# Kernel tuning notes

Hardware: AMD Instinct MI355X
Metric: run time of the kernel (lower is better)

## Reference

```python
import jax, jax.numpy as jnp
import numpy as np

N, E, F, H, L, G, C = 50000, 800000, 64, 128, 4, 64, 10
GAMMA = 10.0  # Gaussian RBF width for centers in (0,1)
CENTERS = jnp.linspace(0.0, 1.0, H)


def _ssp(v):
    # shifted softplus, SchNet's nonlinearity
    return jax.nn.softplus(v) - 0.6931472


def setup_inputs() -> dict:
    key = jax.random.key(0)
    ks = jax.random.split(key, 20)

    def w(k, shape, fan_in):
        return (jax.random.normal(k, shape, dtype=jnp.float32) / np.sqrt(fan_in)).astype(jnp.float32)

    x = jax.random.normal(ks[0], (N, F), dtype=jnp.float32)
    edge_dist = jax.random.uniform(ks[1], (E,), dtype=jnp.float32)
    edge_src = jax.random.randint(ks[2], (E,), 0, N, dtype=jnp.int32)
    edge_dst = jax.random.randint(ks[3], (E,), 0, N, dtype=jnp.int32)
    graph_ids = jnp.sort(jax.random.randint(ks[4], (N,), 0, G, dtype=jnp.int32))

    return {
        "x": x, "edge_dist": edge_dist,
        "edge_src": edge_src, "edge_dst": edge_dst, "graph_ids": graph_ids,
        # first-layer node projection F->H, remaining layers H->H (stacked)
        "W1_0": w(ks[5], (F, H), F), "b1_0": jnp.zeros((H,), jnp.float32),
        "W1_rest": w(ks[6], (L - 1, H, H), H), "b1_rest": jnp.zeros((L - 1, H), jnp.float32),
        # filter-generating MLP on RBF features, per layer
        "Wf1": w(ks[7], (L, H, H), H), "bf1": jnp.zeros((L, H), jnp.float32),
        "Wf2": w(ks[8], (L, H, H), H), "bf2": jnp.zeros((L, H), jnp.float32),
        # output projection per layer
        "W2": w(ks[9], (L, H, H), H), "b2": jnp.zeros((L, H), jnp.float32),
        # readout FC
        "fc_w": w(ks[10], (H, C), H), "fc_b": jnp.zeros((C,), jnp.float32),
    }


def _schnet_conv(x, rbf, src, dst, W1, b1, Wf1, bf1, Wf2, bf2, W2, b2):
    # CFConv: project nodes, gate gathered source features with a distance
    # filter, scatter-sum to destinations, project out.
    filt = _ssp(rbf @ Wf1 + bf1) @ Wf2 + bf2          # [E, H]
    h = x @ W1 + b1                                    # [N, H]
    msg = h[src] * filt                                # [E, H] gather + gate
    agg = jax.ops.segment_sum(msg, dst, num_segments=N)  # [N, H] scatter-sum
    return agg @ W2 + b2


def reference(x, edge_dist, edge_src, edge_dst, graph_ids,
              W1_0, b1_0, W1_rest, b1_rest, Wf1, bf1, Wf2, bf2, W2, b2,
              fc_w, fc_b):
    # Gaussian radial basis expansion of edge distances, shared across layers
    rbf = jnp.exp(-GAMMA * (edge_dist[:, None] - CENTERS) ** 2)  # [E, H]

    h = jax.nn.relu(_schnet_conv(x, rbf, edge_src, edge_dst,
                                 W1_0, b1_0, Wf1[0], bf1[0], Wf2[0], bf2[0],
                                 W2[0], b2[0]))
    for i in range(L - 1):
        h = jax.nn.relu(_schnet_conv(h, rbf, edge_src, edge_dst,
                                     W1_rest[i], b1_rest[i],
                                     Wf1[i + 1], bf1[i + 1],
                                     Wf2[i + 1], bf2[i + 1],
                                     W2[i + 1], b2[i + 1]))

    # dgl.mean_nodes: per-graph mean over nodes
    sums = jax.ops.segment_sum(h, graph_ids, num_segments=G)           # [G, H]
    cnts = jax.ops.segment_sum(jnp.ones((N,), h.dtype), graph_ids, num_segments=G)
    pooled = sums / jnp.maximum(cnts, 1.0)[:, None]

    logits = pooled @ fc_w + fc_b                                       # [G, C]
    return jax.nn.log_softmax(logits, axis=1)
```

## Files before the change

### kernel.cpp

```cpp
#include <hip/hip_runtime.h>
#include <math.h>

#define NN 50000
#define EE 800000
#define FF 64
#define HH 128
#define LL 4
#define GG 64
#define CC 10
#define TT 512
#define TTP 513
#define BD 64
#define ABLK 1024
#define EPB 782
#define SEGC 192
#define SUBB 96
#define SRW 6250

#define PB_CVTW 8
#define PB_TAB ((TT / 16) * LL)
#define PB_CVTX (NN * FF / 4 / 256)
#define PB_PART ABLK

#define SCB (8 * SUBB)
#define GEMMB (NN / 16)

typedef unsigned short ushort_t;
typedef unsigned int uint_t;
typedef unsigned long long u64_t;

typedef short s8v __attribute__((ext_vector_type(8)));
typedef float f32x4 __attribute__((ext_vector_type(4)));

__device__ inline ushort_t f2bf(float f) {
  uint_t u = __float_as_uint(f);
  uint_t r = (u + 0x7FFFu + ((u >> 16) & 1u)) >> 16;
  return (ushort_t)r;
}
__device__ inline float bf1f(ushort_t v) { return __uint_as_float(((uint_t)v) << 16); }

__device__ inline ushort_t f2h(float f) {
  union { _Float16 h[2]; ushort_t us[2]; } c;
  c.h[0] = (_Float16)f;
  return c.us[0];
}
__device__ inline float h_lo(uint_t u) {
  union { uint_t w; _Float16 h[2]; } c; c.w = u; return (float)c.h[0];
}
__device__ inline float h_hi(uint_t u) {
  union { uint_t w; _Float16 h[2]; } c; c.w = u; return (float)c.h[1];
}

__global__ __launch_bounds__(256) void prep(
    const float* __restrict__ x, ushort_t* __restrict__ xb,
    const float* __restrict__ W1_0, const float* __restrict__ W1_rest,
    const float* __restrict__ W2, ushort_t* __restrict__ wt,
    const float* __restrict__ Wf1, const float* __restrict__ bf1,
    const float* __restrict__ Wf2, const float* __restrict__ bf2,
    ushort_t* __restrict__ tables,
    const int* __restrict__ dst, const int* __restrict__ src,
    const float* __restrict__ dist,
    uint_t* __restrict__ seg, int* __restrict__ segcnt, int* __restrict__ bcnt,
    const int* __restrict__ gid, int* __restrict__ gcnt, float* __restrict__ gsum) {
  __shared__ float rbf[16][HH];
  __shared__ float hid[16][HH];
  __shared__ int lcnt[8];
  int tid = threadIdx.x;
  int b = blockIdx.x;

  if (b < PB_CVTW) {
    int mid = b;
    const float* srcm; int K;
    if (mid == 0) { srcm = W1_0; K = FF; }
    else if (mid < 4) { srcm = W1_rest + (size_t)(mid - 1) * HH * HH; K = HH; }
    else { srcm = W2 + (size_t)(mid - 4) * HH * HH; K = HH; }
    ushort_t* dstm = wt + (size_t)mid * HH * HH;
    for (int idx = tid; idx < K * HH; idx += 256) {
      int k = idx >> 7, n = idx & 127;
      __builtin_nontemporal_store(f2bf(srcm[idx]), &dstm[n * K + k]);
    }
  } else if (b < PB_CVTW + PB_TAB) {
    int bb = b - PB_CVTW;
    int l = bb & 3;
    int tb = (bb >> 2) * 16;
    int j = tid & 127;
    float c = j * (1.0f / (HH - 1));
#pragma unroll
    for (int tt2 = 0; tt2 < 16; ++tt2) {
      float d = (tb + tt2) * (1.0f / (TT - 1));
      float dd = d - c;
      rbf[tt2][j] = expf(-10.0f * dd * dd);
    }
    __syncthreads();
    const float* W1f = Wf1 + (size_t)l * HH * HH;
    float s[16];
    float bb1 = bf1[l * HH + j];
#pragma unroll
    for (int tt2 = 0; tt2 < 16; ++tt2) s[tt2] = bb1;
    for (int k = 0; k < HH; ++k) {
      float wk = W1f[(size_t)k * HH + j];
#pragma unroll
      for (int tt2 = 0; tt2 < 16; ++tt2) s[tt2] += rbf[tt2][k] * wk;
    }
#pragma unroll
    for (int tt2 = 0; tt2 < 16; ++tt2)
      hid[tt2][j] = fmaxf(s[tt2], 0.f) + log1pf(expf(-fabsf(s[tt2]))) - 0.6931472f;
    __syncthreads();
    const float* W2f = Wf2 + (size_t)l * HH * HH;
    float bb2 = bf2[l * HH + j];
#pragma unroll
    for (int tt2 = 0; tt2 < 16; ++tt2) s[tt2] = bb2;
    for (int k = 0; k < HH; ++k) {
      float wk = W2f[(size_t)k * HH + j];
#pragma unroll
      for (int tt2 = 0; tt2 < 16; ++tt2) s[tt2] += hid[tt2][k] * wk;
    }
    if (tid < 128) {
#pragma unroll
      for (int tt2 = 0; tt2 < 16; ++tt2)
        __builtin_nontemporal_store(f2h(s[tt2]),
                                    &tables[((size_t)l * TTP + 1 + tb + tt2) * HH + j]);
    }
  } else if (b < PB_CVTW + PB_TAB + PB_CVTX) {
    int i = (b - PB_CVTW - PB_TAB) * 256 + tid;
    const float4* x4 = (const float4*)x;
    float4 v = x4[i];
    union { ushort_t us[4]; u64_t u; } pk;
    pk.us[0] = f2bf(v.x); pk.us[1] = f2bf(v.y); pk.us[2] = f2bf(v.z); pk.us[3] = f2bf(v.w);
    __builtin_nontemporal_store(pk.u, (u64_t*)&xb[i * 4]);
  } else if (b < PB_CVTW + PB_TAB + PB_CVTX + PB_PART) {
    int pb = b - PB_CVTW - PB_TAB - PB_CVTX;
    if (tid < 8) lcnt[tid] = 0;
    int z = pb * 49 + tid;
    if (tid < 49 && z < NN) bcnt[z] = 0;
    __syncthreads();
    int e0 = pb * EPB;
    int e1 = min(e0 + EPB, EE);
    for (int e = e0 + tid; e < e1; e += 256) {
      int d = __builtin_nontemporal_load(dst + e);
      int s = __builtin_nontemporal_load(src + e);
      float di = __builtin_nontemporal_load(dist + e);
      float u = di * (float)(TT - 1);
      int t0 = (int)(fminf(fmaxf(u, 0.f), (float)(TT - 1)) + 0.5f);
      if (t0 > TT - 1) t0 = TT - 1;
      int r = d / SRW;
      int pos = atomicAdd(&lcnt[r], 1);
      if (pos < SEGC) {
        uint_t* sp = seg + (((size_t)(r << 10) + pb) * SEGC + pos) * 2;
        __builtin_nontemporal_store((uint_t)d, sp);
        __builtin_nontemporal_store(((uint_t)s << 10) | (uint_t)(t0 + 1), sp + 1);
      }
    }
    __syncthreads();
    if (tid < 8) segcnt[(tid << 10) + pb] = min(lcnt[tid], SEGC);
  } else {
    for (int i = tid; i < GG * HH; i += 256) gsum[i] = 0.f;
    for (int i = tid; i < LL * HH; i += 256)
      __builtin_nontemporal_store((ushort_t)0,
                                  &tables[(size_t)(i >> 7) * TTP * HH + (i & 127)]);
    if (tid < GG) {
      int g = tid;
      int lo = 0, hi = NN;
      while (lo < hi) { int m = (lo + hi) >> 1; if (gid[m] < g) lo = m + 1; else hi = m; }
      int b0 = lo;
      lo = 0; hi = NN;
      int g1 = g + 1;
      while (lo < hi) { int m = (lo + hi) >> 1; if (gid[m] < g1) lo = m + 1; else hi = m; }
      gcnt[g] = lo - b0;
    }
  }
}

__global__ __launch_bounds__(256) void scatter_gemm1(
    const uint_t* __restrict__ seg, const int* __restrict__ segcnt,
    int* __restrict__ bcnt, uint_t* __restrict__ epad,
    const ushort_t* __restrict__ xb, const ushort_t* __restrict__ wt,
    const float* __restrict__ b1_0, ushort_t* __restrict__ pbuf) {
  int tid = threadIdx.x;
  if (blockIdx.x < SCB) {
    int r = blockIdx.x & 7;
    int sub = blockIdx.x >> 3;
    for (int b = sub; b < ABLK; b += SUBB) {
      int cnt = segcnt[(r << 10) + b];
      const uint_t* sp = seg + ((size_t)(r << 10) + b) * SEGC * 2;
      for (int i = tid; i < cnt; i += 256) {
        uint_t ex = __builtin_nontemporal_load(sp + i * 2);
        uint_t ey = __builtin_nontemporal_load(sp + i * 2 + 1);
        int slot = atomicAdd(&bcnt[ex], 1);
        if (slot < BD) __builtin_nontemporal_store(ey, &epad[(size_t)ex * BD + slot]);
      }
    }
  } else {
    int tile = blockIdx.x - SCB;
    int lane = tid & 63, wave = tid >> 6, m = lane & 15, quad = lane >> 4;
    int rowbase = tile * 16, colbase = wave * 32;
    const ushort_t* arow = xb + (size_t)(rowbase + m) * FF;
    const ushort_t* brow0 = wt + (size_t)(colbase + m) * FF;
    const ushort_t* brow1 = wt + (size_t)(colbase + 16 + m) * FF;
    f32x4 acc0 = {0.f, 0.f, 0.f, 0.f};
    f32x4 acc1 = {0.f, 0.f, 0.f, 0.f};
    for (int kc = 0; kc < FF; kc += 32) {
      int k = kc + quad * 8;
      union { uint4 u; s8v v; } a, b0, b1;
      a.u  = *(const uint4*)(arow + k);
      b0.u = *(const uint4*)(brow0 + k);
      b1.u = *(const uint4*)(brow1 + k);
      acc0 = __builtin_amdgcn_mfma_f32_16x16x32_bf16(a.v, b0.v, acc0, 0, 0, 0);
      acc1 = __builtin_amdgcn_mfma_f32_16x16x32_bf16(a.v, b1.v, acc1, 0, 0, 0);
    }
    float bb0 = b1_0[colbase + m];
    float bb1 = b1_0[colbase + 16 + m];
#pragma unroll
    for (int reg = 0; reg < 4; ++reg) {
      int row = rowbase + quad * 4 + reg;
      __builtin_nontemporal_store(f2h(acc0[reg] + bb0), &pbuf[(size_t)row * HH + colbase + m]);
      __builtin_nontemporal_store(f2h(acc1[reg] + bb1), &pbuf[(size_t)row * HH + colbase + 16 + m]);
    }
  }
}

__global__ __launch_bounds__(512) void fused_layer(
    const ushort_t* __restrict__ pIn, const ushort_t* __restrict__ table,
    const uint_t* __restrict__ epad, const int* __restrict__ bcnt,
    const ushort_t* __restrict__ WT2, const float* __restrict__ b2l,
    const ushort_t* __restrict__ WT1, const float* __restrict__ b1l,
    ushort_t* __restrict__ OUT, int last) {
  __shared__ ushort_t At[16 * 128];
  __shared__ ushort_t T[16 * 128];
  int tid = threadIdx.x;
  int lane = tid & 63;
  int wv = tid >> 6;
  int tile = blockIdx.x;
  const uint_t* pu = (const uint_t*)pIn;
  const uint_t* tu = (const uint_t*)table;

  int baseV = tile * 16 + wv * 2;
  uint_t ed[2];
  float ax[2], ay[2];
  int B = 0;
#pragma unroll
  for (int i = 0; i < 2; ++i) {
    int n = min(bcnt[baseV + i], BD);
    ed[i] = (lane < n) ? epad[(size_t)(baseV + i) * BD + lane] : 0u;
    B = max(B, (n + 3) >> 2);
    ax[i] = 0.f; ay[i] = 0.f;
  }
  for (int c = 0; c < B; ++c) {
    uint_t pv[2][4], fv[2][4];
#pragma unroll
    for (int i = 0; i < 2; ++i) {
#pragma unroll
      for (int k = 0; k < 4; ++k) {
        uint_t e = (uint_t)__builtin_amdgcn_readlane((int)ed[i], c * 4 + k);
        pv[i][k] = pu[(size_t)(e >> 10) * 64 + lane];
        fv[i][k] = tu[(size_t)(e & 1023u) * 64 + lane];
      }
    }
#pragma unroll
    for (int i = 0; i < 2; ++i) {
#pragma unroll
      for (int k = 0; k < 4; ++k) {
        ax[i] += h_lo(pv[i][k]) * h_lo(fv[i][k]);
        ay[i] += h_hi(pv[i][k]) * h_hi(fv[i][k]);
      }
    }
  }
#pragma unroll
  for (int i = 0; i < 2; ++i) {
    int r = wv * 2 + i;
    uint_t packed = (uint_t)f2bf(ax[i]) | ((uint_t)f2bf(ay[i]) << 16);
    ((uint_t*)At)[r * 64 + (((lane >> 2) ^ r) << 2) + (lane & 3)] = packed;
  }
  __syncthreads();
  int m = lane & 15, quad = lane >> 4;
  int rowbase = tile * 16, colbase = wv * 16;
  {
    const ushort_t* brow0 = WT2 + (size_t)(colbase + m) * HH;
    f32x4 acc0 = {0.f, 0.f, 0.f, 0.f};
    for (int kc = 0; kc < HH; kc += 32) {
      int k = kc + quad * 8;
      int g = k >> 3;
      union { uint4 u; s8v v; } a, b0;
      a.u = *(const uint4*)&At[m * 128 + ((g ^ m) << 3)];
      b0.u = *(const uint4*)(brow0 + k);
      acc0 = __builtin_amdgcn_mfma_f32_16x16x32_bf16(a.v, b0.v, acc0, 0, 0, 0);
    }
    float bb0 = b2l[colbase + m];
    if (last) {
#pragma unroll
      for (int reg = 0; reg < 4; ++reg) {
        int row = rowbase + quad * 4 + reg;
        __builtin_nontemporal_store(f2bf(fmaxf(acc0[reg] + bb0, 0.f)),
                                    &OUT[(size_t)row * HH + colbase + m]);
      }
      return;
    }
#pragma unroll
    for (int reg = 0; reg < 4; ++reg) {
      int r = quad * 4 + reg;
      float v0 = fmaxf(acc0[reg] + bb0, 0.f);
      int c0 = colbase + m;
      T[r * 128 + (((c0 >> 3) ^ r) << 3) + (c0 & 7)] = f2bf(v0);
    }
  }
  __syncthreads();
  {
    const ushort_t* brow0 = WT1 + (size_t)(colbase + m) * HH;
    f32x4 acc0 = {0.f, 0.f, 0.f, 0.f};
    for (int kc = 0; kc < HH; kc += 32) {
      int k0 = kc + quad * 8;
      int g = k0 >> 3;
      union { uint4 u; s8v v; } a, b0;
      a.u = *(const uint4*)&T[m * 128 + ((g ^ m) << 3)];
      b0.u = *(const uint4*)(brow0 + k0);
      acc0 = __builtin_amdgcn_mfma_f32_16x16x32_bf16(a.v, b0.v, acc0, 0, 0, 0);
    }
    float bb0 = b1l[colbase + m];
#pragma unroll
    for (int reg = 0; reg < 4; ++reg) {
      int row = rowbase + quad * 4 + reg;
      __builtin_nontemporal_store(f2h(acc0[reg] + bb0),
                                  &OUT[(size_t)row * HH + colbase + m]);
    }
  }
}

__global__ __launch_bounds__(128) void pool_kernel(const ushort_t* __restrict__ h, const int* __restrict__ gid,
                                                   float* __restrict__ gsum) {
  int j = threadIdx.x;
  int i0 = blockIdx.x * 128;
  int i1 = min(i0 + 128, NN);
  if (i0 >= NN) return;
  float acc = 0.f;
  int gcur = gid[i0];
  for (int i = i0; i < i1; ++i) {
    int g = gid[i];
    if (g != gcur) {
      atomicAdd(&gsum[gcur * HH + j], acc);
      acc = 0.f;
      gcur = g;
    }
    acc += bf1f(h[(size_t)i * HH + j]);
  }
  atomicAdd(&gsum[gcur * HH + j], acc);
}

__global__ __launch_bounds__(128) void final_kernel(const float* __restrict__ gsum, const int* __restrict__ gcnt,
                                                    const float* __restrict__ fc_w, const float* __restrict__ fc_b,
                                                    float* __restrict__ out) {
  int g = blockIdx.x, j = threadIdx.x;
  __shared__ float pooled[HH];
  __shared__ float logits[CC];
  __shared__ float lse;
  float cnt = fmaxf((float)gcnt[g], 1.0f);
  pooled[j] = gsum[g * HH + j] / cnt;
  __syncthreads();
  if (j < CC) {
    float s = fc_b[j];
    for (int k = 0; k < HH; ++k) s += pooled[k] * fc_w[k * CC + j];
    logits[j] = s;
  }
  __syncthreads();
  if (j == 0) {
    float m = -1e30f;
    for (int c = 0; c < CC; ++c) m = fmaxf(m, logits[c]);
    float s = 0.f;
    for (int c = 0; c < CC; ++c) s += expf(logits[c] - m);
    lse = m + logf(s);
  }
  __syncthreads();
  if (j < CC) out[g * CC + j] = logits[j] - lse;
}

extern "C" void kernel_launch(void* const* d_in, const int* in_sizes, int n_in,
                              void* d_out, int out_size, void* d_ws, size_t ws_size,
                              hipStream_t stream) {
  const float* x       = (const float*)d_in[0];
  const float* edist   = (const float*)d_in[1];
  const int*   esrc    = (const int*)d_in[2];
  const int*   edst    = (const int*)d_in[3];
  const int*   gid     = (const int*)d_in[4];
  const float* W1_0    = (const float*)d_in[5];
  const float* b1_0    = (const float*)d_in[6];
  const float* W1_rest = (const float*)d_in[7];
  const float* b1_rest = (const float*)d_in[8];
  const float* Wf1     = (const float*)d_in[9];
  const float* bf1     = (const float*)d_in[10];
  const float* Wf2     = (const float*)d_in[11];
  const float* bf2     = (const float*)d_in[12];
  const float* W2      = (const float*)d_in[13];
  const float* b2      = (const float*)d_in[14];
  const float* fc_w    = (const float*)d_in[15];
  const float* fc_b    = (const float*)d_in[16];
  float* out = (float*)d_out;

  char* ws = (char*)d_ws;
  size_t o = 0;
  auto alloc = [&](size_t bytes) {
    void* p = ws + o;
    o += (bytes + 255) & ~(size_t)255;
    return p;
  };
  ushort_t* tables = (ushort_t*)alloc(sizeof(ushort_t) * (size_t)LL * TTP * HH);
  ushort_t* xb     = (ushort_t*)alloc(sizeof(ushort_t) * (size_t)NN * FF);
  ushort_t* wt     = (ushort_t*)alloc(sizeof(ushort_t) * 8 * HH * HH);
  ushort_t* pbuf   = (ushort_t*)alloc(sizeof(ushort_t) * (size_t)NN * HH);
  ushort_t* pbuf2  = (ushort_t*)alloc(sizeof(ushort_t) * (size_t)NN * HH);
  ushort_t* hbuf   = (ushort_t*)alloc(sizeof(ushort_t) * (size_t)NN * HH);
  int*      bcnt   = (int*)alloc(sizeof(int) * NN);
  uint_t*   epad   = (uint_t*)alloc(sizeof(uint_t) * (size_t)NN * BD);
  uint_t*   seg    = (uint_t*)alloc(sizeof(uint_t) * (size_t)2 * 8 * ABLK * SEGC);
  int*      segcnt = (int*)alloc(sizeof(int) * 8 * ABLK);
  float*    gsum   = (float*)alloc(sizeof(float) * GG * HH);
  int*      gcnt   = (int*)alloc(sizeof(int) * GG);

  const int prepBlocks = PB_CVTW + PB_TAB + PB_CVTX + PB_PART + 1;
  prep<<<prepBlocks, 256, 0, stream>>>(x, xb, W1_0, W1_rest, W2, wt,
                                       Wf1, bf1, Wf2, bf2, tables,
                                       edst, esrc, edist, seg, segcnt, bcnt,
                                       gid, gcnt, gsum);
  scatter_gemm1<<<SCB + GEMMB, 256, 0, stream>>>(seg, segcnt, bcnt, epad,
                                                 xb, wt, b1_0, pbuf);

  ushort_t* pIn = pbuf;
  ushort_t* pOut = pbuf2;
  for (int l = 0; l < LL; ++l) {
    int last = (l == LL - 1);
    fused_layer<<<GEMMB, 512, 0, stream>>>(
        pIn, tables + (size_t)l * TTP * HH, epad, bcnt,
        wt + (size_t)(4 + l) * HH * HH, b2 + (size_t)l * HH,
        last ? nullptr : (wt + (size_t)(1 + l) * HH * HH),
        last ? nullptr : (b1_rest + (size_t)l * HH),
        last ? hbuf : pOut, last);
    ushort_t* tmp = pIn; pIn = pOut; pOut = tmp;
  }

  pool_kernel<<<(NN + 127) / 128, 128, 0, stream>>>(hbuf, gid, gsum);
  final_kernel<<<GG, 128, 0, stream>>>(gsum, gcnt, fc_w, fc_b, out);
}
```

Measured before the change: 424.6 us.

## Quantize node features and filter tables to int8 with per-row scales

Node projection outputs and the distance filter tables are stored as int8 with one float scale per row, replacing fp16. This halves the bytes gathered per edge in the message loop. The filter table is shrunk from 512 to 256 distance bins and the edge encoding is adjusted to match. Nontemporal stores are replaced with plain stores. The cost is extra per-row max reductions, scale loads on every edge, and lower numerical precision.

Measured after the change: 436.9 us. 1.03x slower.

```diff
diff --git a/kernel.cpp b/kernel.cpp
--- a/kernel.cpp
+++ b/kernel.cpp
@@ -8,8 +8,8 @@
 #define LL 4
 #define GG 64
 #define CC 10
-#define TT 512
-#define TTP 513
+#define TT 256
+#define TTP 257
 #define BD 64
 #define ABLK 1024
 #define EPB 782
@@ -38,17 +38,10 @@
   return (ushort_t)r;
 }
 __device__ inline float bf1f(ushort_t v) { return __uint_as_float(((uint_t)v) << 16); }
-
 __device__ inline ushort_t f2h(float f) {
   union { _Float16 h[2]; ushort_t us[2]; } c;
   c.h[0] = (_Float16)f;
   return c.us[0];
-}
-__device__ inline float h_lo(uint_t u) {
-  union { uint_t w; _Float16 h[2]; } c; c.w = u; return (float)c.h[0];
-}
-__device__ inline float h_hi(uint_t u) {
-  union { uint_t w; _Float16 h[2]; } c; c.w = u; return (float)c.h[1];
 }
 
 __global__ __launch_bounds__(256) void prep(
@@ -57,7 +50,7 @@
     const float* __restrict__ W2, ushort_t* __restrict__ wt,
     const float* __restrict__ Wf1, const float* __restrict__ bf1,
     const float* __restrict__ Wf2, const float* __restrict__ bf2,
-    ushort_t* __restrict__ tables,
+    char* __restrict__ tabQ, float* __restrict__ tabS,
     const int* __restrict__ dst, const int* __restrict__ src,
     const float* __restrict__ dist,
     uint_t* __restrict__ seg, int* __restrict__ segcnt, int* __restrict__ bcnt,
@@ -65,6 +58,7 @@
   __shared__ float rbf[16][HH];
   __shared__ float hid[16][HH];
   __shared__ int lcnt[8];
+  __shared__ uint_t rmx[16];
   int tid = threadIdx.x;
   int b = blockIdx.x;
 
@@ -77,13 +71,14 @@
     ushort_t* dstm = wt + (size_t)mid * HH * HH;
     for (int idx = tid; idx < K * HH; idx += 256) {
       int k = idx >> 7, n = idx & 127;
-      __builtin_nontemporal_store(f2bf(srcm[idx]), &dstm[n * K + k]);
+      dstm[n * K + k] = f2bf(srcm[idx]);
     }
   } else if (b < PB_CVTW + PB_TAB) {
     int bb = b - PB_CVTW;
     int l = bb & 3;
     int tb = (bb >> 2) * 16;
     int j = tid & 127;
+    if (tid < 16) rmx[tid] = 0u;
     float c = j * (1.0f / (HH - 1));
 #pragma unroll
     for (int tt2 = 0; tt2 < 16; ++tt2) {
@@ -118,16 +113,25 @@
     if (tid < 128) {
 #pragma unroll
       for (int tt2 = 0; tt2 < 16; ++tt2)
-        __builtin_nontemporal_store(f2h(s[tt2]),
-                                    &tables[((size_t)l * TTP + 1 + tb + tt2) * HH + j]);
-    }
+        atomicMax(&rmx[tt2], __float_as_uint(fabsf(s[tt2])));
+    }
+    __syncthreads();
+    if (tid < 128) {
+#pragma unroll
+      for (int tt2 = 0; tt2 < 16; ++tt2) {
+        float inv = 127.0f / fmaxf(__uint_as_float(rmx[tt2]), 1e-30f);
+        tabQ[((size_t)l * TTP + 1 + tb + tt2) * HH + j] = (char)(int)rintf(s[tt2] * inv);
+      }
+    }
+    if (tid < 16)
+      tabS[(size_t)l * TTP + 1 + tb + tid] = __uint_as_float(rmx[tid]) * (1.0f / 127.0f);
   } else if (b < PB_CVTW + PB_TAB + PB_CVTX) {
     int i = (b - PB_CVTW - PB_TAB) * 256 + tid;
     const float4* x4 = (const float4*)x;
     float4 v = x4[i];
     union { ushort_t us[4]; u64_t u; } pk;
     pk.us[0] = f2bf(v.x); pk.us[1] = f2bf(v.y); pk.us[2] = f2bf(v.z); pk.us[3] = f2bf(v.w);
-    __builtin_nontemporal_store(pk.u, (u64_t*)&xb[i * 4]);
+    *(u64_t*)&xb[i * 4] = pk.u;
   } else if (b < PB_CVTW + PB_TAB + PB_CVTX + PB_PART) {
     int pb = b - PB_CVTW - PB_TAB - PB_CVTX;
     if (tid < 8) lcnt[tid] = 0;
@@ -147,8 +151,8 @@
       int pos = atomicAdd(&lcnt[r], 1);
       if (pos < SEGC) {
         uint_t* sp = seg + (((size_t)(r << 10) + pb) * SEGC + pos) * 2;
-        __builtin_nontemporal_store((uint_t)d, sp);
-        __builtin_nontemporal_store(((uint_t)s << 10) | (uint_t)(t0 + 1), sp + 1);
+        sp[0] = (uint_t)d;
+        sp[1] = ((uint_t)s << 9) | (uint_t)(t0 + 1);
       }
     }
     __syncthreads();
@@ -156,10 +160,10 @@
   } else {
     for (int i = tid; i < GG * HH; i += 256) gsum[i] = 0.f;
     for (int i = tid; i < LL * HH; i += 256)
-      __builtin_nontemporal_store((ushort_t)0,
-                                  &tables[(size_t)(i >> 7) * TTP * HH + (i & 127)]);
-    if (tid < GG) {
-      int g = tid;
+      tabQ[(size_t)(i >> 7) * TTP * HH + (i & 127)] = 0;
+    if (tid < LL) tabS[(size_t)tid * TTP] = 0.f;
+    if (tid >= 32 && tid < 32 + GG) {
+      int g = tid - 32;
       int lo = 0, hi = NN;
       while (lo < hi) { int m = (lo + hi) >> 1; if (gid[m] < g) lo = m + 1; else hi = m; }
       int b0 = lo;
@@ -175,7 +179,9 @@
     const uint_t* __restrict__ seg, const int* __restrict__ segcnt,
     int* __restrict__ bcnt, uint_t* __restrict__ epad,
     const ushort_t* __restrict__ xb, const ushort_t* __restrict__ wt,
-    const float* __restrict__ b1_0, ushort_t* __restrict__ pbuf) {
+    const float* __restrict__ b1_0, char* __restrict__ q8Out,
+    float* __restrict__ sclOut) {
+  __shared__ uint_t rmaxL[16];
   int tid = threadIdx.x;
   if (blockIdx.x < SCB) {
     int r = blockIdx.x & 7;
@@ -187,10 +193,11 @@
         uint_t ex = __builtin_nontemporal_load(sp + i * 2);
         uint_t ey = __builtin_nontemporal_load(sp + i * 2 + 1);
         int slot = atomicAdd(&bcnt[ex], 1);
-        if (slot < BD) __builtin_nontemporal_store(ey, &epad[(size_t)ex * BD + slot]);
+        if (slot < BD) epad[(size_t)ex * BD + slot] = ey;
       }
     }
   } else {
+    if (tid < 16) rmaxL[tid] = 0u;
     int tile = blockIdx.x - SCB;
     int lane = tid & 63, wave = tid >> 6, m = lane & 15, quad = lane >> 4;
     int rowbase = tile * 16, colbase = wave * 32;
@@ -210,29 +217,46 @@
     }
     float bb0 = b1_0[colbase + m];
     float bb1 = b1_0[colbase + 16 + m];
+    float v0r[4], v1r[4];
 #pragma unroll
     for (int reg = 0; reg < 4; ++reg) {
-      int row = rowbase + quad * 4 + reg;
-      __builtin_nontemporal_store(f2h(acc0[reg] + bb0), &pbuf[(size_t)row * HH + colbase + m]);
-      __builtin_nontemporal_store(f2h(acc1[reg] + bb1), &pbuf[(size_t)row * HH + colbase + 16 + m]);
-    }
+      v0r[reg] = acc0[reg] + bb0;
+      v1r[reg] = acc1[reg] + bb1;
+      int r = quad * 4 + reg;
+      atomicMax(&rmaxL[r], __float_as_uint(fmaxf(fabsf(v0r[reg]), fabsf(v1r[reg]))));
+    }
+    __syncthreads();
+#pragma unroll
+    for (int reg = 0; reg < 4; ++reg) {
+      int r = quad * 4 + reg;
+      int row = rowbase + r;
+      float inv = 127.0f / fmaxf(__uint_as_float(rmaxL[r]), 1e-30f);
+      q8Out[(size_t)row * HH + colbase + m] = (char)(int)rintf(v0r[reg] * inv);
+      q8Out[(size_t)row * HH + colbase + 16 + m] = (char)(int)rintf(v1r[reg] * inv);
+    }
+    if (tid < 16) sclOut[rowbase + tid] = __uint_as_float(rmaxL[tid]) * (1.0f / 127.0f);
   }
 }
 
 __global__ __launch_bounds__(512) void fused_layer(
-    const ushort_t* __restrict__ pIn, const ushort_t* __restrict__ table,
+    const char* __restrict__ q8In, const float* __restrict__ sclIn,
+    const char* __restrict__ tabQ, const float* __restrict__ tabS,
     const uint_t* __restrict__ epad, const int* __restrict__ bcnt,
     const ushort_t* __restrict__ WT2, const float* __restrict__ b2l,
     const ushort_t* __restrict__ WT1, const float* __restrict__ b1l,
-    ushort_t* __restrict__ OUT, int last) {
+    char* __restrict__ q8Out, float* __restrict__ sclOut,
+    ushort_t* __restrict__ hbuf, int last) {
   __shared__ ushort_t At[16 * 128];
   __shared__ ushort_t T[16 * 128];
+  __shared__ uint_t rmaxL[16];
   int tid = threadIdx.x;
   int lane = tid & 63;
   int wv = tid >> 6;
   int tile = blockIdx.x;
-  const uint_t* pu = (const uint_t*)pIn;
-  const uint_t* tu = (const uint_t*)table;
+  if (tid < 16) rmaxL[tid] = 0u;
+
+  const ushort_t* pq = (const ushort_t*)q8In;
+  const ushort_t* tq = (const ushort_t*)tabQ;
 
   int baseV = tile * 16 + wv * 2;
   uint_t ed[2];
@@ -247,21 +271,28 @@
   }
   for (int c = 0; c < B; ++c) {
     uint_t pv[2][4], fv[2][4];
+    float sc[2][4];
 #pragma unroll
     for (int i = 0; i < 2; ++i) {
 #pragma unroll
       for (int k = 0; k < 4; ++k) {
         uint_t e = (uint_t)__builtin_amdgcn_readlane((int)ed[i], c * 4 + k);
-        pv[i][k] = pu[(size_t)(e >> 10) * 64 + lane];
-        fv[i][k] = tu[(size_t)(e & 1023u) * 64 + lane];
+        pv[i][k] = pq[(size_t)(e >> 9) * 64 + lane];
+        fv[i][k] = tq[(size_t)(e & 511u) * 64 + lane];
+        sc[i][k] = sclIn[e >> 9] * tabS[e & 511u];
       }
     }
 #pragma unroll
     for (int i = 0; i < 2; ++i) {
 #pragma unroll
       for (int k = 0; k < 4; ++k) {
-        ax[i] += h_lo(pv[i][k]) * h_lo(fv[i][k]);
-        ay[i] += h_hi(pv[i][k]) * h_hi(fv[i][k]);
+        int wp = (int)pv[i][k], wf = (int)fv[i][k];
+        float p0 = (float)((wp << 24) >> 24);
+        float p1 = (float)((wp << 16) >> 24);
+        float f0 = (float)((wf << 24) >> 24);
+        float f1 = (float)((wf << 16) >> 24);
+        ax[i] += (p0 * f0) * sc[i][k];
+        ay[i] += (p1 * f1) * sc[i][k];
       }
     }
   }
@@ -290,8 +321,7 @@
 #pragma unroll
       for (int reg = 0; reg < 4; ++reg) {
         int row = rowbase + quad * 4 + reg;
-        __builtin_nontemporal_store(f2bf(fmaxf(acc0[reg] + bb0, 0.f)),
-                                    &OUT[(size_t)row * HH + colbase + m]);
+        hbuf[(size_t)row * HH + colbase + m] = f2bf(fmaxf(acc0[reg] + bb0, 0.f));
       }
       return;
     }
@@ -316,12 +346,22 @@
       acc0 = __builtin_amdgcn_mfma_f32_16x16x32_bf16(a.v, b0.v, acc0, 0, 0, 0);
     }
     float bb0 = b1l[colbase + m];
+    float v0r[4];
 #pragma unroll
     for (int reg = 0; reg < 4; ++reg) {
-      int row = rowbase + quad * 4 + reg;
-      __builtin_nontemporal_store(f2h(acc0[reg] + bb0),
-                                  &OUT[(size_t)row * HH + colbase + m]);
-    }
+      v0r[reg] = acc0[reg] + bb0;
+      int r = quad * 4 + reg;
+      atomicMax(&rmaxL[r], __float_as_uint(fabsf(v0r[reg])));
+    }
+    __syncthreads();
+#pragma unroll
+    for (int reg = 0; reg < 4; ++reg) {
+      int r = quad * 4 + reg;
+      int row = rowbase + r;
+      float inv = 127.0f / fmaxf(__uint_as_float(rmaxL[r]), 1e-30f);
+      q8Out[(size_t)row * HH + colbase + m] = (char)(int)rintf(v0r[reg] * inv);
+    }
+    if (tid < 16) sclOut[rowbase + tid] = __uint_as_float(rmaxL[tid]) * (1.0f / 127.0f);
   }
 }
 
@@ -401,11 +441,14 @@
     o += (bytes + 255) & ~(size_t)255;
     return p;
   };
-  ushort_t* tables = (ushort_t*)alloc(sizeof(ushort_t) * (size_t)LL * TTP * HH);
+  char*     tabQ   = (char*)alloc(sizeof(char) * (size_t)LL * TTP * HH);
+  float*    tabS   = (float*)alloc(sizeof(float) * (size_t)LL * TTP);
   ushort_t* xb     = (ushort_t*)alloc(sizeof(ushort_t) * (size_t)NN * FF);
   ushort_t* wt     = (ushort_t*)alloc(sizeof(ushort_t) * 8 * HH * HH);
-  ushort_t* pbuf   = (ushort_t*)alloc(sizeof(ushort_t) * (size_t)NN * HH);
-  ushort_t* pbuf2  = (ushort_t*)alloc(sizeof(ushort_t) * (size_t)NN * HH);
+  char*     q8a    = (char*)alloc(sizeof(char) * (size_t)NN * HH);
+  char*     q8b    = (char*)alloc(sizeof(char) * (size_t)NN * HH);
+  float*    scla   = (float*)alloc(sizeof(float) * (size_t)NN);
+  float*    sclb   = (float*)alloc(sizeof(float) * (size_t)NN);
   ushort_t* hbuf   = (ushort_t*)alloc(sizeof(ushort_t) * (size_t)NN * HH);
   int*      bcnt   = (int*)alloc(sizeof(int) * NN);
   uint_t*   epad   = (uint_t*)alloc(sizeof(uint_t) * (size_t)NN * BD);
@@ -416,23 +459,27 @@
 
   const int prepBlocks = PB_CVTW + PB_TAB + PB_CVTX + PB_PART + 1;
   prep<<<prepBlocks, 256, 0, stream>>>(x, xb, W1_0, W1_rest, W2, wt,
-                                       Wf1, bf1, Wf2, bf2, tables,
+                                       Wf1, bf1, Wf2, bf2, tabQ, tabS,
                                        edst, esrc, edist, seg, segcnt, bcnt,
                                        gid, gcnt, gsum);
   scatter_gemm1<<<SCB + GEMMB, 256, 0, stream>>>(seg, segcnt, bcnt, epad,
-                                                 xb, wt, b1_0, pbuf);
-
-  ushort_t* pIn = pbuf;
-  ushort_t* pOut = pbuf2;
+                                                 xb, wt, b1_0, q8a, scla);
+
+  const char* pIn = q8a;
+  const float* sIn = scla;
+  char* pOut = q8b;
+  float* sOut = sclb;
   for (int l = 0; l < LL; ++l) {
     int last = (l == LL - 1);
     fused_layer<<<GEMMB, 512, 0, stream>>>(
-        pIn, tables + (size_t)l * TTP * HH, epad, bcnt,
+        pIn, sIn, tabQ + (size_t)l * TTP * HH, tabS + (size_t)l * TTP,
+        epad, bcnt,
         wt + (size_t)(4 + l) * HH * HH, b2 + (size_t)l * HH,
         last ? nullptr : (wt + (size_t)(1 + l) * HH * HH),
         last ? nullptr : (b1_rest + (size_t)l * HH),
-        last ? hbuf : pOut, last);
-    ushort_t* tmp = pIn; pIn = pOut; pOut = tmp;
+        pOut, sOut, hbuf, last);
+    const char* tp = pIn; pIn = pOut; pOut = (char*)tp;
+    const float* ts = sIn; sIn = sOut; sOut = (float*)ts;
   }
 
   pool_kernel<<<(NN + 127) / 128, 128, 0, stream>>>(hbuf, gid, gsum);
```
